# Performance work log

Measured on AMD Instinct MI355X. Metric: run time of the kernel, lower is better.

Reference implementation:

```python
import jax, jax.numpy as jnp
import numpy as np

N_NODES = 100000
N_EDGES = 1600000
IN_DIM = 128
OUT_DIM = 128


def setup_inputs() -> dict:
    key = jax.random.key(0)
    k1, k2, k3, k4, k5 = jax.random.split(key, 5)
    x = jax.random.normal(k1, (N_NODES, IN_DIM), dtype=jnp.float32)
    edge_index = jax.random.randint(k2, (2, N_EDGES), 0, N_NODES, dtype=jnp.int64)
    s = 1.0 / np.sqrt(IN_DIM)
    # PyG SAGEConv params: lin_l (neighbor branch, with bias), lin_r (root branch, no bias)
    W_l = jax.random.uniform(k3, (OUT_DIM, IN_DIM), jnp.float32, -s, s)
    b_l = jax.random.uniform(k4, (OUT_DIM,), jnp.float32, -s, s)
    W_r = jax.random.uniform(k5, (OUT_DIM, IN_DIM), jnp.float32, -s, s)
    return {"x": x, "edge_index": edge_index, "W_l": W_l, "b_l": b_l, "W_r": W_r}


def reference(x, edge_index, W_l, b_l, W_r):
    src = edge_index[0]  # message source j
    dst = edge_index[1]  # aggregation target i
    # mean aggregation of neighbor features at each target node
    msg_sum = jax.ops.segment_sum(x[src], dst, num_segments=N_NODES)  # [N, in]
    deg = jax.ops.segment_sum(jnp.ones((N_EDGES,), x.dtype), dst, num_segments=N_NODES)
    agg = msg_sum / jnp.maximum(deg, 1.0)[:, None]
    # out = lin_l(agg) + lin_r(x)
    out = agg @ W_l.T + b_l + x @ W_r.T  # [N, out]
    # L2 normalize (F.normalize, p=2, dim=-1, eps=1e-12)
    norm = jnp.sqrt(jnp.sum(out * out, axis=-1, keepdims=True))
    out = out / jnp.maximum(norm, 1e-12)
    return out
```

## Files before the change

kernel.cpp:

```cpp
#include <hip/hip_runtime.h>
#include <hip/hip_fp16.h>
#include <stdint.h>

#define NN 100000
#define D 128
#define W0 128
#define NB ((NN + W0 - 1) / W0)
#define C1 4096
#define LDS_E 3072

typedef _Float16 f16x8 __attribute__((ext_vector_type(8)));
typedef float f32x4 __attribute__((ext_vector_type(4)));

static const size_t O_FLAG   = 0;
static const size_t O_BCNT   = 256;
static const size_t O_BSTART = O_BCNT + 4096;
static const size_t O_BCUR   = O_BSTART + 4096;
static const size_t O_WTL    = O_BCUR + 4096;
static const size_t O_WTR    = O_WTL + (size_t)D * D * 4;
static const size_t O_OFFS   = O_WTR + (size_t)D * D * 4;
static const size_t O_DEG    = O_OFFS + (size_t)(NN + 64) * 4;
static const size_t O_RECS   = O_DEG + (size_t)NN * 4;

__device__ __forceinline__ int edge_at(const int* ei, long long pos, int is64) {
    return is64 ? ei[2 * pos] : ei[pos];
}

__device__ __forceinline__ int detect_is64(const int* __restrict__ ei, long long E,
                                           int t, int* s_is64) {
    if (t < 64) {
        int bad = 0;
        if (t < E)      bad |= (ei[2 * t + 1] != 0);
        if (t + 64 < E) bad |= (ei[2 * (t + 64) + 1] != 0);
        unsigned long long m = __ballot(bad);
        if (t == 0) *s_is64 = (m == 0ull) ? 1 : 0;
    }
    return 0;
}


__global__ __launch_bounds__(256) void k_prep(
        const float* __restrict__ x, const int* __restrict__ ei,
        const float* __restrict__ Wl, const float* __restrict__ Wr,
        __half* __restrict__ xh, __half* __restrict__ Bp,
        int* __restrict__ bhist, long long E)
{
    __shared__ int cnt[NB];
    __shared__ int s_is64;
    int t = threadIdx.x, b = blockIdx.x;
    detect_is64(ei, E, t, &s_is64);
    for (int i = t; i < NB; i += 256) cnt[i] = 0;
    __syncthreads();
    int is64 = s_is64;

    int idx = b * 256 + t;
    if (idx < 32768) {
        int j  = idx & 7;
        int l  = (idx >> 3) & 63;
        int tt = (idx >> 9) & 7;
        int s  = idx >> 12;
        int col = tt * 16 + (l & 15);
        int k   = s * 32 + (l >> 4) * 8 + j;
        float v = (k < 128) ? Wl[col * 128 + k] : Wr[col * 128 + (k - 128)];
        Bp[idx] = __float2half_rn(v);
    }
    const long long n4 = (long long)NN * D / 4;
    for (long long i = (long long)b * 256 + t; i < n4; i += (long long)gridDim.x * 256) {
        float4 v = ((const float4*)x)[i];
        ((__half2*)xh)[2 * i]     = __floats2half2_rn(v.x, v.y);
        ((__half2*)xh)[2 * i + 1] = __floats2half2_rn(v.z, v.w);
    }
    long long base = (long long)b * C1;
    for (int j = t; j < C1; j += 256) {
        long long e = base + j;
        if (e < E) atomicAdd(&cnt[edge_at(ei, E + e, is64) >> 7], 1);
    }
    __syncthreads();
    for (int i = t; i < NB; i += 256)
        bhist[(long long)b * NB + i] = cnt[i];
}

__global__ __launch_bounds__(1024) void k_scan(const int* __restrict__ bhist,
                                               int* __restrict__ bstart,
                                               int* __restrict__ bcur, int pb)
{
    __shared__ int sh[1024];
    int t = threadIdx.x;
    int sum = 0;
    if (t < NB) {
#pragma unroll 8
        for (int c = 0; c < pb; ++c) sum += bhist[(long long)c * NB + t];
    }
    sh[t] = sum;
    __syncthreads();
    for (int d = 1; d < 1024; d <<= 1) {
        int v = (t >= d) ? sh[t - d] : 0;
        __syncthreads();
        sh[t] += v;
        __syncthreads();
    }
    if (t < NB) {
        int ex = (t > 0) ? sh[t - 1] : 0;
        bstart[t] = ex;
        bcur[t] = ex;
    }
    if (t == NB - 1) bstart[NB] = sh[NB - 1];
}

__global__ __launch_bounds__(256) void k_scat(const int* __restrict__ ei,
                                              int* __restrict__ bcur,
                                              const int* __restrict__ bhist,
                                              unsigned int* __restrict__ recs,
                                              long long E)
{
    __shared__ int cnt[NB];
    __shared__ int rbase[NB];
    __shared__ int s_is64;
    int t = threadIdx.x, b = blockIdx.x;
    detect_is64(ei, E, t, &s_is64);
    __syncthreads();
    int is64 = s_is64;
    const int* h = bhist + (long long)b * NB;
    for (int i = t; i < NB; i += 256) {
        int c = h[i];
        rbase[i] = c ? atomicAdd(&bcur[i], c) : 0;
        cnt[i] = 0;
    }
    __syncthreads();
    long long base = (long long)b * C1;
    for (int j = t; j < C1; j += 256) {
        long long e = base + j;
        if (e < E) {
            int s = edge_at(ei, e, is64);
            int d = edge_at(ei, E + e, is64);
            int bu = d >> 7;
            int pos = rbase[bu] + atomicAdd(&cnt[bu], 1);
            recs[pos] = (unsigned)s | ((unsigned)(d & (W0 - 1)) << 20);
        }
    }
}

__global__ __launch_bounds__(512) void k_p2agg(const unsigned int* __restrict__ recs,
                                               const int* __restrict__ bstart,
                                               const __half* __restrict__ xh,
                                               int* __restrict__ srcs,
                                               __half* __restrict__ aggh, int N)
{
    __shared__ int cnt[W0];
    __shared__ int off[W0];
    __shared__ int sl[LDS_E];
    int t = threadIdx.x, b = blockIdx.x;
    int e0 = bstart[b], e1 = bstart[b + 1];
    int ne = e1 - e0;
    bool fits = (ne <= LDS_E);

    if (t < W0) cnt[t] = 0;
    __syncthreads();
    for (int e = e0 + t; e < e1; e += 512)
        atomicAdd(&cnt[recs[e] >> 20], 1);
    __syncthreads();
    if (t < W0) off[t] = cnt[t];
    __syncthreads();
    for (int d = 1; d < W0; d <<= 1) {
        int v = 0;
        if (t < W0 && t >= d) v = off[t - d];
        __syncthreads();
        if (t < W0) off[t] += v;
        __syncthreads();
    }
    if (t < W0) cnt[t] = (t > 0) ? off[t - 1] : 0;
    __syncthreads();
    for (int e = e0 + t; e < e1; e += 512) {
        unsigned r = recs[e];
        int pos = atomicAdd(&cnt[r >> 20], 1);
        if (fits) sl[pos] = (int)(r & 0xFFFFFu);
        else      srcs[e0 + pos] = (int)(r & 0xFFFFFu);
    }
    __syncthreads();

    int lane = t & 63;
    int wid  = t >> 6;
    const __half2* x2 = (const __half2*)xh;

    auto run = [&](auto getsrc) {
        for (int i = 0; i < 16; ++i) {
            int n = wid * 16 + i;
            int node = b * W0 + n;
            if (node >= N) break;
            int s0 = (n > 0) ? off[n - 1] : 0;
            int s1 = off[n];
            float ax = 0.f, ay = 0.f;
            int e = s0;
            for (; e + 8 <= s1; e += 8) {
                int ss[8];
#pragma unroll
                for (int u = 0; u < 8; ++u) ss[u] = getsrc(e + u);
                __half2 h[8];
#pragma unroll
                for (int u = 0; u < 8; ++u) h[u] = x2[(long long)ss[u] * 64 + lane];
#pragma unroll
                for (int u = 0; u < 8; ++u) {
                    float2 v = __half22float2(h[u]);
                    ax += v.x; ay += v.y;
                }
            }
            for (; e + 2 <= s1; e += 2) {
                int sa = getsrc(e), sb = getsrc(e + 1);
                float2 v0 = __half22float2(x2[(long long)sa * 64 + lane]);
                float2 v1 = __half22float2(x2[(long long)sb * 64 + lane]);
                ax += v0.x + v1.x;
                ay += v0.y + v1.y;
            }
            if (e < s1) {
                float2 v = __half22float2(x2[(long long)getsrc(e) * 64 + lane]);
                ax += v.x; ay += v.y;
            }
            float inv = 1.0f / fmaxf((float)(s1 - s0), 1.0f);
            ((__half2*)aggh)[(long long)node * 64 + lane] =
                __floats2half2_rn(ax * inv, ay * inv);
        }
    };
    if (fits) run([&](int e) { return sl[e]; });
    else      run([&](int e) { return srcs[e0 + e]; });
}

__global__ __launch_bounds__(256) void k_gemm_m(const __half* __restrict__ aggh,
                                                const __half* __restrict__ xh,
                                                const __half* __restrict__ Bp,
                                                const float* __restrict__ bl,
                                                float* __restrict__ out, int N) {
    __shared__ __half Bs[32768];
    int t = threadIdx.x;
#pragma unroll
    for (int i = 0; i < 16; ++i) {
        int idx = t + i * 256;
        ((float4*)Bs)[idx] = ((const float4*)Bp)[idx];
    }
    int lane = t & 63;
    int wid  = t >> 6;
    int row0 = blockIdx.x * 128 + wid * 32;
    int rA = row0 + (lane & 15);
    int rB = rA + 16;
    long long ra = (rA < N) ? rA : (N - 1);
    long long rb = (rB < N) ? rB : (N - 1);
    int koff = (lane >> 4) * 8;

    f32x4 acc[2][8];
#pragma unroll
    for (int r = 0; r < 2; ++r)
#pragma unroll
        for (int c = 0; c < 8; ++c)
            acc[r][c] = (f32x4){0.f, 0.f, 0.f, 0.f};

    __syncthreads();

#pragma unroll
    for (int s = 0; s < 8; ++s) {
        const __half* Ap = (s < 4) ? aggh : xh;
        int kb = (s & 3) * 32 + koff;
        f16x8 a0 = *(const f16x8*)(Ap + ra * 128 + kb);
        f16x8 a1 = *(const f16x8*)(Ap + rb * 128 + kb);
        const __half* bs = Bs + s * 4096 + lane * 8;
#pragma unroll
        for (int tt = 0; tt < 8; ++tt) {
            f16x8 b = *(const f16x8*)(bs + tt * 512);
            acc[0][tt] = __builtin_amdgcn_mfma_f32_16x16x32_f16(a0, b, acc[0][tt], 0, 0, 0);
            acc[1][tt] = __builtin_amdgcn_mfma_f32_16x16x32_f16(a1, b, acc[1][tt], 0, 0, 0);
        }
    }

    float bias[8];
#pragma unroll
    for (int tt = 0; tt < 8; ++tt) bias[tt] = bl[tt * 16 + (lane & 15)];

#pragma unroll
    for (int rt = 0; rt < 2; ++rt) {
#pragma unroll
        for (int r = 0; r < 4; ++r) {
            int row = row0 + rt * 16 + (lane >> 4) * 4 + r;
            float v[8];
            float ss = 0.f;
#pragma unroll
            for (int tt = 0; tt < 8; ++tt) {
                v[tt] = acc[rt][tt][r] + bias[tt];
                ss = fmaf(v[tt], v[tt], ss);
            }
            ss += __shfl_xor(ss, 1, 64);
            ss += __shfl_xor(ss, 2, 64);
            ss += __shfl_xor(ss, 4, 64);
            ss += __shfl_xor(ss, 8, 64);
            float scale = 1.0f / fmaxf(sqrtf(ss), 1e-12f);
            if (row < N) {
                float* op = out + (long long)row * D + (lane & 15);
#pragma unroll
                for (int tt = 0; tt < 8; ++tt)
                    op[tt * 16] = v[tt] * scale;
            }
        }
    }
}

__global__ void k_detect(const int* __restrict__ ei, int* flag, long long E) {
    int l = threadIdx.x;
    int bad = 0;
    if (l < E)       bad |= (ei[2 * l + 1] != 0);
    if (l + 64 < E)  bad |= (ei[2 * (l + 64) + 1] != 0);
    unsigned long long m = __ballot(bad);
    if (l == 0) *flag = (m == 0ull) ? 1 : 0;
}

__global__ void k_transpose(const float* __restrict__ Wl, const float* __restrict__ Wr,
                            float* __restrict__ WtL, float* __restrict__ WtR) {
    int t = blockIdx.x * 256 + threadIdx.x;
    if (t < D * D) {
        int o = t >> 7, k = t & 127;
        WtL[k * D + o] = Wl[t];
        WtR[k * D + o] = Wr[t];
    }
}

__global__ __launch_bounds__(256) void k_p1count(const int* __restrict__ ei,
                                                 const int* __restrict__ flag,
                                                 int* __restrict__ bcount, long long E) {
    __shared__ int cnt[NB];
    for (int i = threadIdx.x; i < NB; i += 256) cnt[i] = 0;
    __syncthreads();
    int is64 = *flag;
    long long base = (long long)blockIdx.x * C1;
    for (int j = threadIdx.x; j < C1; j += 256) {
        long long e = base + j;
        if (e < E) atomicAdd(&cnt[edge_at(ei, E + e, is64) >> 7], 1);
    }
    __syncthreads();
    for (int i = threadIdx.x; i < NB; i += 256) {
        int c = cnt[i];
        if (c) atomicAdd(&bcount[i], c);
    }
}

__global__ __launch_bounds__(1024) void k_bscan(const int* __restrict__ bcount,
                                                int* __restrict__ bstart,
                                                int* __restrict__ bcur,
                                                int* __restrict__ offs) {
    __shared__ int sh[1024];
    int t = threadIdx.x;
    sh[t] = (t < NB) ? bcount[t] : 0;
    __syncthreads();
    for (int d = 1; d < 1024; d <<= 1) {
        int v = (t >= d) ? sh[t - d] : 0;
        __syncthreads();
        sh[t] += v;
        __syncthreads();
    }
    if (t < NB) {
        int ex = (t > 0) ? sh[t - 1] : 0;
        bstart[t] = ex;
        bcur[t] = ex;
    }
    if (t == NB - 1) {
        bstart[NB] = sh[NB - 1];
        offs[NN] = sh[NB - 1];
    }
}

__global__ __launch_bounds__(256) void k_p1scatter(const int* __restrict__ ei,
                                                   const int* __restrict__ flag,
                                                   int* __restrict__ bcur,
                                                   unsigned int* __restrict__ recs,
                                                   long long E) {
    __shared__ int cnt[NB];
    __shared__ int rbase[NB];
    for (int i = threadIdx.x; i < NB; i += 256) cnt[i] = 0;
    __syncthreads();
    int is64 = *flag;
    long long base = (long long)blockIdx.x * C1;
    for (int j = threadIdx.x; j < C1; j += 256) {
        long long e = base + j;
        if (e < E) atomicAdd(&cnt[edge_at(ei, E + e, is64) >> 7], 1);
    }
    __syncthreads();
    for (int i = threadIdx.x; i < NB; i += 256) {
        int c = cnt[i];
        rbase[i] = c ? atomicAdd(&bcur[i], c) : 0;
    }
    __syncthreads();
    for (int i = threadIdx.x; i < NB; i += 256) cnt[i] = 0;
    __syncthreads();
    for (int j = threadIdx.x; j < C1; j += 256) {
        long long e = base + j;
        if (e < E) {
            int s = edge_at(ei, e, is64);
            int d = edge_at(ei, E + e, is64);
            int bu = d >> 7;
            int pos = rbase[bu] + atomicAdd(&cnt[bu], 1);
            recs[pos] = (unsigned)s | ((unsigned)(d & (W0 - 1)) << 20);
        }
    }
}

__global__ __launch_bounds__(256) void k_p2(const unsigned int* __restrict__ recs,
                                            const int* __restrict__ bstart,
                                            int* __restrict__ offs,
                                            int* __restrict__ srcs, int N) {
    __shared__ int cnt[W0];
    __shared__ int off[W0];
    int t = threadIdx.x;
    int bu = blockIdx.x;
    int e0 = bstart[bu], e1 = bstart[bu + 1];
    if (t < W0) cnt[t] = 0;
    __syncthreads();
    for (int e = e0 + t; e < e1; e += 256)
        atomicAdd(&cnt[recs[e] >> 20], 1);
    __syncthreads();
    if (t < W0) off[t] = cnt[t];
    __syncthreads();
    for (int d = 1; d < W0; d <<= 1) {
        int v = 0;
        if (t < W0 && t >= d) v = off[t - d];
        __syncthreads();
        if (t < W0) off[t] += v;
        __syncthreads();
    }
    if (t < W0) {
        int ex = (t > 0) ? off[t - 1] : 0;
        int node = bu * W0 + t;
        if (node < N) offs[node] = e0 + ex;
        cnt[t] = e0 + ex;
    }
    __syncthreads();
    for (int e = e0 + t; e < e1; e += 256) {
        unsigned r = recs[e];
        int pos = atomicAdd(&cnt[r >> 20], 1);
        srcs[pos] = (int)(r & 0xFFFFFu);
    }
}

__global__ __launch_bounds__(256) void k_agg(const float* __restrict__ x,
                                             const int* __restrict__ offs,
                                             const int* __restrict__ srcs,
                                             float* agg, int N) {
    int lane = threadIdx.x & 63;
    int wid = __builtin_amdgcn_readfirstlane(threadIdx.x >> 6);
    int node = blockIdx.x * 4 + wid;
    if (node >= N) return;
    int e0 = offs[node], e1 = offs[node + 1];
    const float2* x2 = (const float2*)x;
    float ax = 0.f, ay = 0.f;
    int e = e0;
    for (; e + 4 <= e1; e += 4) {
        int s0 = srcs[e], s1 = srcs[e + 1], s2 = srcs[e + 2], s3 = srcs[e + 3];
        float2 v0 = x2[(long long)s0 * 64 + lane];
        float2 v1 = x2[(long long)s1 * 64 + lane];
        float2 v2 = x2[(long long)s2 * 64 + lane];
        float2 v3 = x2[(long long)s3 * 64 + lane];
        ax += v0.x + v1.x + v2.x + v3.x;
        ay += v0.y + v1.y + v2.y + v3.y;
    }
    for (; e < e1; ++e) {
        int s = srcs[e];
        float2 v = x2[(long long)s * 64 + lane];
        ax += v.x; ay += v.y;
    }
    float inv = 1.0f / fmaxf((float)(e1 - e0), 1.0f);
    float2 o; o.x = ax * inv; o.y = ay * inv;
    ((float2*)agg)[(long long)node * 64 + lane] = o;
}

__global__ __launch_bounds__(256) void k_scatterB(const float* __restrict__ x,
                                                  const int* __restrict__ ei,
                                                  const int* __restrict__ flag,
                                                  float* out, float* deg, long long E) {
    int lane = threadIdx.x & 63;
    long long e = (long long)blockIdx.x * 4 + (threadIdx.x >> 6);
    if (e >= E) return;
    int is64 = *flag;
    int s = edge_at(ei, e, is64);
    int d = edge_at(ei, E + e, is64);
    atomicAdd(&out[(long long)d * D + lane], x[(long long)s * D + lane]);
    atomicAdd(&out[(long long)d * D + 64 + lane], x[(long long)s * D + 64 + lane]);
    if (lane == 0) atomicAdd(&deg[d], 1.0f);
}

__global__ void k_meanB(float* out, const float* __restrict__ deg) {
    long long i = (long long)blockIdx.x * 256 + threadIdx.x;
    if (i >= (long long)NN * D) return;
    out[i] *= 1.0f / fmaxf(deg[i >> 7], 1.0f);
}

__global__ __launch_bounds__(256) void k_gemm(const float* __restrict__ x,
                                              const float* agg,
                                              const float* __restrict__ WtL,
                                              const float* __restrict__ WtR,
                                              const float* __restrict__ bl,
                                              float* out, int N) {
    __shared__ float Bs[64 * D];
    int t = threadIdx.x;
    int tx = t & 15;
    int ty = t >> 4;
    int row0 = blockIdx.x * 64 + ty * 4;
    int c0a = tx * 4;
    int c0b = 64 + tx * 4;

    float acc[4][8];
    float4 b0 = *(const float4*)(bl + c0a);
    float4 b1 = *(const float4*)(bl + c0b);
#pragma unroll
    for (int r = 0; r < 4; ++r) {
        acc[r][0] = b0.x; acc[r][1] = b0.y; acc[r][2] = b0.z; acc[r][3] = b0.w;
        acc[r][4] = b1.x; acc[r][5] = b1.y; acc[r][6] = b1.z; acc[r][7] = b1.w;
    }

    long long rws[4];
#pragma unroll
    for (int r = 0; r < 4; ++r) {
        int rr = row0 + r;
        rws[r] = (rr < N) ? (long long)rr : (long long)(N - 1);
    }

    for (int phase = 0; phase < 2; ++phase) {
        const float* A = phase ? x : agg;
        const float* W = phase ? WtR : WtL;
        const float4* Ar0 = (const float4*)(A + rws[0] * D);
        const float4* Ar1 = (const float4*)(A + rws[1] * D);
        const float4* Ar2 = (const float4*)(A + rws[2] * D);
        const float4* Ar3 = (const float4*)(A + rws[3] * D);

        for (int half = 0; half < 2; ++half) {
            if (phase | half) __syncthreads();
#pragma unroll
            for (int i = 0; i < 8; ++i) {
                int idx = t + i * 256;
                ((float4*)Bs)[idx] = ((const float4*)(W + half * 64 * D))[idx];
            }
            __syncthreads();

#pragma unroll 2
            for (int k4 = 0; k4 < 16; ++k4) {
                int ak4 = half * 16 + k4;
                float4 av[4];
                av[0] = Ar0[ak4]; av[1] = Ar1[ak4]; av[2] = Ar2[ak4]; av[3] = Ar3[ak4];
#pragma unroll
                for (int kk = 0; kk < 4; ++kk) {
                    int k = k4 * 4 + kk;
                    float4 w0 = *(const float4*)&Bs[k * D + c0a];
                    float4 w1 = *(const float4*)&Bs[k * D + c0b];
#pragma unroll
                    for (int r = 0; r < 4; ++r) {
                        float a = (kk == 0) ? av[r].x : (kk == 1) ? av[r].y
                                 : (kk == 2) ? av[r].z : av[r].w;
                        acc[r][0] = fmaf(a, w0.x, acc[r][0]);
                        acc[r][1] = fmaf(a, w0.y, acc[r][1]);
                        acc[r][2] = fmaf(a, w0.z, acc[r][2]);
                        acc[r][3] = fmaf(a, w0.w, acc[r][3]);
                        acc[r][4] = fmaf(a, w1.x, acc[r][4]);
                        acc[r][5] = fmaf(a, w1.y, acc[r][5]);
                        acc[r][6] = fmaf(a, w1.z, acc[r][6]);
                        acc[r][7] = fmaf(a, w1.w, acc[r][7]);
                    }
                }
            }
        }
    }

#pragma unroll
    for (int r = 0; r < 4; ++r) {
        float s = 0.f;
#pragma unroll
        for (int j = 0; j < 8; ++j) s = fmaf(acc[r][j], acc[r][j], s);
        s += __shfl_xor(s, 1, 64);
        s += __shfl_xor(s, 2, 64);
        s += __shfl_xor(s, 4, 64);
        s += __shfl_xor(s, 8, 64);
        float scale = 1.0f / fmaxf(sqrtf(s), 1e-12f);
        int rr = row0 + r;
        if (rr < N) {
            float4 v0, v1;
            v0.x = acc[r][0] * scale; v0.y = acc[r][1] * scale;
            v0.z = acc[r][2] * scale; v0.w = acc[r][3] * scale;
            v1.x = acc[r][4] * scale; v1.y = acc[r][5] * scale;
            v1.z = acc[r][6] * scale; v1.w = acc[r][7] * scale;
            float* op = out + (long long)rr * D;
            *(float4*)(op + c0a) = v0;
            *(float4*)(op + c0b) = v1;
        }
    }
}

extern "C" void kernel_launch(void* const* d_in, const int* in_sizes, int n_in,
                              void* d_out, int out_size, void* d_ws, size_t ws_size,
                              hipStream_t stream) {
    const float* x  = (const float*)d_in[0];
    const int*   ei = (const int*)d_in[1];
    const float* Wl = (const float*)d_in[2];
    const float* bl = (const float*)d_in[3];
    const float* Wr = (const float*)d_in[4];
    float* out = (float*)d_out;
    const long long E = (long long)in_sizes[1] / 2;

    char* ws = (char*)d_ws;
    int*      flag   = (int*)(ws + O_FLAG);
    int*      bcount = (int*)(ws + O_BCNT);
    int*      bstart = (int*)(ws + O_BSTART);
    int*      bcur   = (int*)(ws + O_BCUR);
    float*    WtL    = (float*)(ws + O_WTL);
    float*    WtR    = (float*)(ws + O_WTR);
    __half*   Bph    = (__half*)(ws + O_WTL);
    int*      offs   = (int*)(ws + O_OFFS);
    float*    deg    = (float*)(ws + O_DEG);
    unsigned* recs   = (unsigned*)(ws + O_RECS);
    int*      srcs   = (int*)(ws + O_RECS + (size_t)E * 4);
    const size_t O_XH = O_RECS + (size_t)E * 8;
    __half*   xh     = (__half*)(ws + O_XH);
    const size_t O_AGGH = O_XH + (size_t)NN * D * 2;
    __half*   aggh   = (__half*)(ws + O_AGGH);
    const size_t O_BHIST = O_AGGH + (size_t)NN * D * 2;
    int*      bhist  = (int*)(ws + O_BHIST);

    int pb = (int)((E + C1 - 1) / C1);
    size_t planA_bytes = O_RECS + (size_t)E * 8;
    size_t fast_bytes  = O_BHIST + (size_t)pb * NB * 4;
    bool planA = ws_size >= planA_bytes;
    bool useF  = ws_size >= fast_bytes;

    if (useF) {
        k_prep<<<pb, 256, 0, stream>>>(x, ei, Wl, Wr, xh, Bph, bhist, E);
        k_scan<<<1, 1024, 0, stream>>>(bhist, bstart, bcur, pb);
        k_scat<<<pb, 256, 0, stream>>>(ei, bcur, bhist, recs, E);
        k_p2agg<<<NB, 512, 0, stream>>>(recs, bstart, xh, srcs, aggh, NN);
        k_gemm_m<<<(NN + 127) / 128, 256, 0, stream>>>(aggh, xh, Bph, bl, out, NN);
        return;
    }

    k_detect<<<1, 64, 0, stream>>>(ei, flag, E);
    k_transpose<<<(D * D + 255) / 256, 256, 0, stream>>>(Wl, Wr, WtL, WtR);

    if (planA) {
        hipMemsetAsync(ws + O_BCNT, 0, (size_t)NB * 4, stream);
        k_p1count<<<pb, 256, 0, stream>>>(ei, flag, bcount, E);
        k_bscan<<<1, 1024, 0, stream>>>(bcount, bstart, bcur, offs);
        k_p1scatter<<<pb, 256, 0, stream>>>(ei, flag, bcur, recs, E);
        k_p2<<<NB, 256, 0, stream>>>(recs, bstart, offs, srcs, NN);
        k_agg<<<(NN + 3) / 4, 256, 0, stream>>>(x, offs, srcs, out, NN);
    } else {
        hipMemsetAsync(out, 0, (size_t)NN * D * 4, stream);
        hipMemsetAsync(ws + O_DEG, 0, (size_t)NN * 4, stream);
        k_scatterB<<<(int)((E + 3) / 4), 256, 0, stream>>>(x, ei, flag, out, deg, E);
        k_meanB<<<(int)(((long long)NN * D + 255) / 256), 256, 0, stream>>>(out, deg);
    }
    k_gemm<<<(NN + 63) / 64, 256, 0, stream>>>(x, out, WtL, WtR, bl, out, NN);
}
```

Measured before the change: 265.3 us.

## Fuse bucketing into one pass with fixed-capacity buckets and fuse aggregation with GEMM

Replaces the histogram, scan and scatter kernels with a single build kernel. It writes edge records into fixed-capacity per-bucket slots (CAP per 128-node bucket) using atomic cursors, and sends any excess to a small global overflow list. The aggregation kernel now keeps the mean features in LDS and runs the MFMA GEMM and L2 normalization itself, so the fp16 agg buffer is never written to or read from global memory. The costs are more per-bucket atomics on global cursors, a linear scan of the overflow list per node, and larger LDS use per block, which may lower occupancy.

```diff
diff --git a/kernel.cpp b/kernel.cpp
--- a/kernel.cpp
+++ b/kernel.cpp
@@ -7,7 +7,8 @@
 #define W0 128
 #define NB ((NN + W0 - 1) / W0)
 #define C1 4096
-#define LDS_E 3072
+#define CAP 4096
+#define OVF_CAP 65536
 
 typedef _Float16 f16x8 __attribute__((ext_vector_type(8)));
 typedef float f32x4 __attribute__((ext_vector_type(4)));
@@ -21,13 +22,15 @@
 static const size_t O_OFFS   = O_WTR + (size_t)D * D * 4;
 static const size_t O_DEG    = O_OFFS + (size_t)(NN + 64) * 4;
 static const size_t O_RECS   = O_DEG + (size_t)NN * 4;
+static const size_t O_OVF    = O_RECS + (size_t)NB * CAP * 4;
+static const size_t O_XH     = O_OVF + (size_t)OVF_CAP * 8;
 
 __device__ __forceinline__ int edge_at(const int* ei, long long pos, int is64) {
     return is64 ? ei[2 * pos] : ei[pos];
 }
 
-__device__ __forceinline__ int detect_is64(const int* __restrict__ ei, long long E,
-                                           int t, int* s_is64) {
+__device__ __forceinline__ void detect_is64(const int* __restrict__ ei, long long E,
+                                            int t, int* s_is64) {
     if (t < 64) {
         int bad = 0;
         if (t < E)      bad |= (ei[2 * t + 1] != 0);
@@ -35,17 +38,18 @@
         unsigned long long m = __ballot(bad);
         if (t == 0) *s_is64 = (m == 0ull) ? 1 : 0;
     }
-    return 0;
-}
-
-
-__global__ __launch_bounds__(256) void k_prep(
+}
+
+__global__ __launch_bounds__(256) void k_build(
         const float* __restrict__ x, const int* __restrict__ ei,
         const float* __restrict__ Wl, const float* __restrict__ Wr,
         __half* __restrict__ xh, __half* __restrict__ Bp,
-        int* __restrict__ bhist, long long E)
+        int* __restrict__ bcur, int* __restrict__ ovf_cnt,
+        unsigned long long* __restrict__ ovf,
+        unsigned int* __restrict__ recs, long long E)
 {
     __shared__ int cnt[NB];
+    __shared__ int rbase[NB];
     __shared__ int s_is64;
     int t = threadIdx.x, b = blockIdx.x;
     detect_is64(ei, E, t, &s_is64);
@@ -76,88 +80,51 @@
         if (e < E) atomicAdd(&cnt[edge_at(ei, E + e, is64) >> 7], 1);
     }
     __syncthreads();
-    for (int i = t; i < NB; i += 256)
-        bhist[(long long)b * NB + i] = cnt[i];
-}
-
-__global__ __launch_bounds__(1024) void k_scan(const int* __restrict__ bhist,
-                                               int* __restrict__ bstart,
-                                               int* __restrict__ bcur, int pb)
-{
-    __shared__ int sh[1024];
-    int t = threadIdx.x;
-    int sum = 0;
-    if (t < NB) {
-#pragma unroll 8
-        for (int c = 0; c < pb; ++c) sum += bhist[(long long)c * NB + t];
-    }
-    sh[t] = sum;
-    __syncthreads();
-    for (int d = 1; d < 1024; d <<= 1) {
-        int v = (t >= d) ? sh[t - d] : 0;
-        __syncthreads();
-        sh[t] += v;
-        __syncthreads();
-    }
-    if (t < NB) {
-        int ex = (t > 0) ? sh[t - 1] : 0;
-        bstart[t] = ex;
-        bcur[t] = ex;
-    }
-    if (t == NB - 1) bstart[NB] = sh[NB - 1];
-}
-
-__global__ __launch_bounds__(256) void k_scat(const int* __restrict__ ei,
-                                              int* __restrict__ bcur,
-                                              const int* __restrict__ bhist,
-                                              unsigned int* __restrict__ recs,
-                                              long long E)
-{
-    __shared__ int cnt[NB];
-    __shared__ int rbase[NB];
-    __shared__ int s_is64;
-    int t = threadIdx.x, b = blockIdx.x;
-    detect_is64(ei, E, t, &s_is64);
-    __syncthreads();
-    int is64 = s_is64;
-    const int* h = bhist + (long long)b * NB;
     for (int i = t; i < NB; i += 256) {
-        int c = h[i];
+        int c = cnt[i];
         rbase[i] = c ? atomicAdd(&bcur[i], c) : 0;
         cnt[i] = 0;
     }
     __syncthreads();
-    long long base = (long long)b * C1;
     for (int j = t; j < C1; j += 256) {
         long long e = base + j;
         if (e < E) {
             int s = edge_at(ei, e, is64);
             int d = edge_at(ei, E + e, is64);
             int bu = d >> 7;
+            unsigned rec = (unsigned)s | ((unsigned)(d & (W0 - 1)) << 20);
             int pos = rbase[bu] + atomicAdd(&cnt[bu], 1);
-            recs[pos] = (unsigned)s | ((unsigned)(d & (W0 - 1)) << 20);
-        }
-    }
-}
-
-__global__ __launch_bounds__(512) void k_p2agg(const unsigned int* __restrict__ recs,
-                                               const int* __restrict__ bstart,
-                                               const __half* __restrict__ xh,
-                                               int* __restrict__ srcs,
-                                               __half* __restrict__ aggh, int N)
+            if (pos < CAP) recs[(long long)bu * CAP + pos] = rec;
+            else {
+                int op = atomicAdd(ovf_cnt, 1);
+                if (op < OVF_CAP) ovf[op] = ((unsigned long long)bu << 32) | rec;
+            }
+        }
+    }
+}
+
+__global__ __launch_bounds__(512) void k_p2agg_g(
+        const unsigned int* __restrict__ recs,
+        const int* __restrict__ bcur, const int* __restrict__ ovf_cnt,
+        const unsigned long long* __restrict__ ovf,
+        const __half* __restrict__ xh, const __half* __restrict__ Bp,
+        const float* __restrict__ bl, float* __restrict__ out, int N)
 {
     __shared__ int cnt[W0];
     __shared__ int off[W0];
-    __shared__ int sl[LDS_E];
+    __shared__ int sl[CAP];
+    __shared__ __half aw[8][16][136];
+    __shared__ int s_oc;
     int t = threadIdx.x, b = blockIdx.x;
-    int e0 = bstart[b], e1 = bstart[b + 1];
-    int ne = e1 - e0;
-    bool fits = (ne <= LDS_E);
+    long long e0g = (long long)b * CAP;
+    int ne = bcur[b];
+    if (ne > CAP) ne = CAP;
+    if (t == 0) s_oc = min(*ovf_cnt, OVF_CAP);
 
     if (t < W0) cnt[t] = 0;
     __syncthreads();
-    for (int e = e0 + t; e < e1; e += 512)
-        atomicAdd(&cnt[recs[e] >> 20], 1);
+    for (int e = t; e < ne; e += 512)
+        atomicAdd(&cnt[recs[e0g + e] >> 20], 1);
     __syncthreads();
     if (t < W0) off[t] = cnt[t];
     __syncthreads();
@@ -170,102 +137,82 @@
     }
     if (t < W0) cnt[t] = (t > 0) ? off[t - 1] : 0;
     __syncthreads();
-    for (int e = e0 + t; e < e1; e += 512) {
-        unsigned r = recs[e];
+    for (int e = t; e < ne; e += 512) {
+        unsigned r = recs[e0g + e];
         int pos = atomicAdd(&cnt[r >> 20], 1);
-        if (fits) sl[pos] = (int)(r & 0xFFFFFu);
-        else      srcs[e0 + pos] = (int)(r & 0xFFFFFu);
+        sl[pos] = (int)(r & 0xFFFFFu);
     }
     __syncthreads();
 
     int lane = t & 63;
     int wid  = t >> 6;
+    int oc   = s_oc;
     const __half2* x2 = (const __half2*)xh;
 
-    auto run = [&](auto getsrc) {
-        for (int i = 0; i < 16; ++i) {
-            int n = wid * 16 + i;
-            int node = b * W0 + n;
-            if (node >= N) break;
-            int s0 = (n > 0) ? off[n - 1] : 0;
-            int s1 = off[n];
-            float ax = 0.f, ay = 0.f;
-            int e = s0;
-            for (; e + 8 <= s1; e += 8) {
-                int ss[8];
-#pragma unroll
-                for (int u = 0; u < 8; ++u) ss[u] = getsrc(e + u);
-                __half2 h[8];
-#pragma unroll
-                for (int u = 0; u < 8; ++u) h[u] = x2[(long long)ss[u] * 64 + lane];
-#pragma unroll
-                for (int u = 0; u < 8; ++u) {
-                    float2 v = __half22float2(h[u]);
-                    ax += v.x; ay += v.y;
+    for (int i = 0; i < 16; ++i) {
+        int n = wid * 16 + i;
+        int node = b * W0 + n;
+        if (node >= N) break;
+        int s0 = (n > 0) ? off[n - 1] : 0;
+        int s1 = off[n];
+        float ax = 0.f, ay = 0.f;
+        int e = s0;
+        for (; e + 8 <= s1; e += 8) {
+            int ss[8];
+#pragma unroll
+            for (int u = 0; u < 8; ++u) ss[u] = sl[e + u];
+            __half2 h[8];
+#pragma unroll
+            for (int u = 0; u < 8; ++u) h[u] = x2[(long long)ss[u] * 64 + lane];
+#pragma unroll
+            for (int u = 0; u < 8; ++u) {
+                float2 v = __half22float2(h[u]);
+                ax += v.x; ay += v.y;
+            }
+        }
+        for (; e + 2 <= s1; e += 2) {
+            int sa = sl[e], sb = sl[e + 1];
+            float2 v0 = __half22float2(x2[(long long)sa * 64 + lane]);
+            float2 v1 = __half22float2(x2[(long long)sb * 64 + lane]);
+            ax += v0.x + v1.x;
+            ay += v0.y + v1.y;
+        }
+        if (e < s1) {
+            float2 v = __half22float2(x2[(long long)sl[e] * 64 + lane]);
+            ax += v.x; ay += v.y;
+        }
+        int extra = 0;
+        for (int k = 0; k < oc; ++k) {
+            unsigned long long v = ovf[k];
+            if ((int)(v >> 32) == b) {
+                unsigned rec = (unsigned)v;
+                if ((int)(rec >> 20) == n) {
+                    float2 w = __half22float2(x2[(long long)(rec & 0xFFFFFu) * 64 + lane]);
+                    ax += w.x; ay += w.y; ++extra;
                 }
             }
-            for (; e + 2 <= s1; e += 2) {
-                int sa = getsrc(e), sb = getsrc(e + 1);
-                float2 v0 = __half22float2(x2[(long long)sa * 64 + lane]);
-                float2 v1 = __half22float2(x2[(long long)sb * 64 + lane]);
-                ax += v0.x + v1.x;
-                ay += v0.y + v1.y;
-            }
-            if (e < s1) {
-                float2 v = __half22float2(x2[(long long)getsrc(e) * 64 + lane]);
-                ax += v.x; ay += v.y;
-            }
-            float inv = 1.0f / fmaxf((float)(s1 - s0), 1.0f);
-            ((__half2*)aggh)[(long long)node * 64 + lane] =
-                __floats2half2_rn(ax * inv, ay * inv);
-        }
-    };
-    if (fits) run([&](int e) { return sl[e]; });
-    else      run([&](int e) { return srcs[e0 + e]; });
-}
-
-__global__ __launch_bounds__(256) void k_gemm_m(const __half* __restrict__ aggh,
-                                                const __half* __restrict__ xh,
-                                                const __half* __restrict__ Bp,
-                                                const float* __restrict__ bl,
-                                                float* __restrict__ out, int N) {
-    __shared__ __half Bs[32768];
-    int t = threadIdx.x;
-#pragma unroll
-    for (int i = 0; i < 16; ++i) {
-        int idx = t + i * 256;
-        ((float4*)Bs)[idx] = ((const float4*)Bp)[idx];
-    }
-    int lane = t & 63;
-    int wid  = t >> 6;
-    int row0 = blockIdx.x * 128 + wid * 32;
-    int rA = row0 + (lane & 15);
-    int rB = rA + 16;
-    long long ra = (rA < N) ? rA : (N - 1);
-    long long rb = (rB < N) ? rB : (N - 1);
+        }
+        float inv = 1.0f / fmaxf((float)(s1 - s0 + extra), 1.0f);
+        *(__half2*)&aw[wid][i][2 * lane] = __floats2half2_rn(ax * inv, ay * inv);
+    }
+
+    f32x4 acc[8];
+#pragma unroll
+    for (int c = 0; c < 8; ++c) acc[c] = (f32x4){0.f, 0.f, 0.f, 0.f};
+
+    int rn = b * W0 + wid * 16 + (lane & 15);
+    long long rx = (rn < N) ? rn : (N - 1);
     int koff = (lane >> 4) * 8;
-
-    f32x4 acc[2][8];
-#pragma unroll
-    for (int r = 0; r < 2; ++r)
-#pragma unroll
-        for (int c = 0; c < 8; ++c)
-            acc[r][c] = (f32x4){0.f, 0.f, 0.f, 0.f};
-
-    __syncthreads();
-
 #pragma unroll
     for (int s = 0; s < 8; ++s) {
-        const __half* Ap = (s < 4) ? aggh : xh;
-        int kb = (s & 3) * 32 + koff;
-        f16x8 a0 = *(const f16x8*)(Ap + ra * 128 + kb);
-        f16x8 a1 = *(const f16x8*)(Ap + rb * 128 + kb);
-        const __half* bs = Bs + s * 4096 + lane * 8;
+        f16x8 a;
+        if (s < 4) a = *(const f16x8*)&aw[wid][lane & 15][s * 32 + koff];
+        else       a = *(const f16x8*)(xh + rx * 128 + (s & 3) * 32 + koff);
+        const __half* bp = Bp + ((s * 8) * 64 + lane) * 8;
 #pragma unroll
         for (int tt = 0; tt < 8; ++tt) {
-            f16x8 b = *(const f16x8*)(bs + tt * 512);
-            acc[0][tt] = __builtin_amdgcn_mfma_f32_16x16x32_f16(a0, b, acc[0][tt], 0, 0, 0);
-            acc[1][tt] = __builtin_amdgcn_mfma_f32_16x16x32_f16(a1, b, acc[1][tt], 0, 0, 0);
+            f16x8 bf = *(const f16x8*)(bp + tt * 512);
+            acc[tt] = __builtin_amdgcn_mfma_f32_16x16x32_f16(a, bf, acc[tt], 0, 0, 0);
         }
     }
 
@@ -274,28 +221,26 @@
     for (int tt = 0; tt < 8; ++tt) bias[tt] = bl[tt * 16 + (lane & 15)];
 
 #pragma unroll
-    for (int rt = 0; rt < 2; ++rt) {
-#pragma unroll
-        for (int r = 0; r < 4; ++r) {
-            int row = row0 + rt * 16 + (lane >> 4) * 4 + r;
-            float v[8];
-            float ss = 0.f;
-#pragma unroll
-            for (int tt = 0; tt < 8; ++tt) {
-                v[tt] = acc[rt][tt][r] + bias[tt];
-                ss = fmaf(v[tt], v[tt], ss);
-            }
-            ss += __shfl_xor(ss, 1, 64);
-            ss += __shfl_xor(ss, 2, 64);
-            ss += __shfl_xor(ss, 4, 64);
-            ss += __shfl_xor(ss, 8, 64);
-            float scale = 1.0f / fmaxf(sqrtf(ss), 1e-12f);
-            if (row < N) {
-                float* op = out + (long long)row * D + (lane & 15);
-#pragma unroll
-                for (int tt = 0; tt < 8; ++tt)
-                    op[tt * 16] = v[tt] * scale;
-            }
+    for (int r = 0; r < 4; ++r) {
+        int n = (lane >> 4) * 4 + r;
+        int node = b * W0 + wid * 16 + n;
+        float v[8];
+        float ss = 0.f;
+#pragma unroll
+        for (int tt = 0; tt < 8; ++tt) {
+            v[tt] = acc[tt][r] + bias[tt];
+            ss = fmaf(v[tt], v[tt], ss);
+        }
+        ss += __shfl_xor(ss, 1, 64);
+        ss += __shfl_xor(ss, 2, 64);
+        ss += __shfl_xor(ss, 4, 64);
+        ss += __shfl_xor(ss, 8, 64);
+        float scale = 1.0f / fmaxf(sqrtf(ss), 1e-12f);
+        if (node < N) {
+            float* op = out + (long long)node * D + (lane & 15);
+#pragma unroll
+            for (int tt = 0; tt < 8; ++tt)
+                op[tt * 16] = v[tt] * scale;
         }
     }
 }
@@ -602,6 +547,7 @@
     int*      bcount = (int*)(ws + O_BCNT);
     int*      bstart = (int*)(ws + O_BSTART);
     int*      bcur   = (int*)(ws + O_BCUR);
+    int*      ovfc   = (int*)(ws + O_BCUR + 3200);
     float*    WtL    = (float*)(ws + O_WTL);
     float*    WtR    = (float*)(ws + O_WTR);
     __half*   Bph    = (__half*)(ws + O_WTL);
@@ -609,25 +555,19 @@
     float*    deg    = (float*)(ws + O_DEG);
     unsigned* recs   = (unsigned*)(ws + O_RECS);
     int*      srcs   = (int*)(ws + O_RECS + (size_t)E * 4);
-    const size_t O_XH = O_RECS + (size_t)E * 8;
+    unsigned long long* ovf = (unsigned long long*)(ws + O_OVF);
     __half*   xh     = (__half*)(ws + O_XH);
-    const size_t O_AGGH = O_XH + (size_t)NN * D * 2;
-    __half*   aggh   = (__half*)(ws + O_AGGH);
-    const size_t O_BHIST = O_AGGH + (size_t)NN * D * 2;
-    int*      bhist  = (int*)(ws + O_BHIST);
 
     int pb = (int)((E + C1 - 1) / C1);
     size_t planA_bytes = O_RECS + (size_t)E * 8;
-    size_t fast_bytes  = O_BHIST + (size_t)pb * NB * 4;
+    size_t fast_bytes  = O_XH + (size_t)NN * D * 2;
     bool planA = ws_size >= planA_bytes;
-    bool useF  = ws_size >= fast_bytes;
+    bool useF  = (ws_size >= fast_bytes) && (E <= (long long)NB * CAP);
 
     if (useF) {
-        k_prep<<<pb, 256, 0, stream>>>(x, ei, Wl, Wr, xh, Bph, bhist, E);
-        k_scan<<<1, 1024, 0, stream>>>(bhist, bstart, bcur, pb);
-        k_scat<<<pb, 256, 0, stream>>>(ei, bcur, bhist, recs, E);
-        k_p2agg<<<NB, 512, 0, stream>>>(recs, bstart, xh, srcs, aggh, NN);
-        k_gemm_m<<<(NN + 127) / 128, 256, 0, stream>>>(aggh, xh, Bph, bl, out, NN);
+        hipMemsetAsync(ws + O_BCUR, 0, 4096, stream);
+        k_build<<<pb, 256, 0, stream>>>(x, ei, Wl, Wr, xh, Bph, bcur, ovfc, ovf, recs, E);
+        k_p2agg_g<<<NB, 512, 0, stream>>>(recs, bcur, ovfc, ovf, xh, Bph, bl, out, NN);
         return;
     }
 
```

Measured after the change: 246.4 us. 1.08x faster.
